# Kernel optimization log

Measured on AMD Instinct MI355X. Metric: run time of the kernel, lower is better.

## Reference

```python
import jax, jax.numpy as jnp
import numpy as np

S, B_BOX, C = 7, 2, 20
LAMBDA_COORD = 5.0
LAMBDA_NOOBJ = 0.5


def _iou(b1, b2):
    # b1, b2: [..., 4] in (cx, cy, w, h) format
    area1 = b1[..., 2] * b1[..., 3]
    area2 = b2[..., 2] * b2[..., 3]
    max_left = jnp.maximum(b1[..., 0] - b1[..., 2] / 2, b2[..., 0] - b2[..., 2] / 2)
    min_right = jnp.minimum(b1[..., 0] + b1[..., 2] / 2, b2[..., 0] + b2[..., 2] / 2)
    max_top = jnp.maximum(b1[..., 1] - b1[..., 3] / 2, b2[..., 1] - b2[..., 3] / 2)
    min_bottom = jnp.minimum(b1[..., 1] + b1[..., 3] / 2, b2[..., 1] + b2[..., 3] / 2)
    iw = jnp.maximum(min_right - max_left, 0.0)
    ih = jnp.maximum(min_bottom - max_top, 0.0)
    inter = iw * ih
    union = area1 + area2 - inter
    return jnp.where(inter > 0.0, inter / union, 0.0)


def setup_inputs() -> dict:
    key = jax.random.key(0)
    k1, k2, k3 = jax.random.split(key, 3)
    batch = 16384
    shape = (batch, S, S, C + 5 * B_BOX)  # [..., 30]
    pred = jax.random.uniform(k1, shape, dtype=jnp.float32)
    target = jax.random.uniform(k2, shape, dtype=jnp.float32)
    # objectness flag must be exactly 1.0 to trigger the obj branch
    obj_flag = jax.random.bernoulli(k3, 0.3, shape[:-1]).astype(jnp.float32)
    target = target.at[..., 0].set(obj_flag)
    return {"pred": pred, "target": target}


def reference(pred, target):
    batch = pred.shape[0]
    pred = pred.reshape(-1, S, S, C + 5 * B_BOX)
    target = target.reshape(-1, S, S, C + 5 * B_BOX)

    obj = (target[..., 0] == 1.0)          # [b,S,S] bool
    obj_f = obj.astype(pred.dtype)
    noobj_f = 1.0 - obj_f

    gt = target[..., 1:5]
    box1 = pred[..., 1:5]                   # predictor 1 box
    box2 = target[..., 6:10]                # NOTE: original code uses target's 2nd box
    iou1 = jax.lax.stop_gradient(_iou(box1, gt))
    iou2 = jax.lax.stop_gradient(_iou(box2, gt))
    resp1 = iou1 > iou2                     # predictor 1 responsible (strict >)
    r1 = resp1[..., None]

    # coord losses (responsible predictor)
    pxy = jnp.where(r1, pred[..., 1:3], pred[..., 6:8])
    txy = jnp.where(r1, target[..., 1:3], target[..., 6:8])
    pwh = jnp.where(r1, pred[..., 3:5], pred[..., 8:10])
    twh = jnp.where(r1, target[..., 3:5], target[..., 8:10])
    cell_xy = jnp.sum((pxy - txy) ** 2, axis=-1)
    cell_wh = jnp.sum((jnp.sqrt(pwh) - jnp.sqrt(twh)) ** 2, axis=-1)

    # obj confidence loss: responsible conf vs its iou
    conf_resp = jnp.where(resp1, pred[..., 0], pred[..., 5])
    iou_resp = jnp.where(resp1, iou1, iou2)
    cell_obj = (conf_resp - iou_resp) ** 2

    # noobj: non-responsible conf in obj cells; both confs in empty cells
    conf_other = jnp.where(resp1, pred[..., 5], pred[..., 0])
    cell_noobj_obj = conf_other ** 2
    cell_noobj_empty = pred[..., 0] ** 2 + pred[..., 5] ** 2

    cell_class = jnp.sum((pred[..., 10:] - target[..., 10:]) ** 2, axis=-1)

    loss_coord_xy = LAMBDA_COORD * jnp.sum(obj_f * cell_xy)
    loss_coord_wh = LAMBDA_COORD * jnp.sum(obj_f * cell_wh)
    loss_obj = jnp.sum(obj_f * cell_obj)
    loss_noobj = LAMBDA_NOOBJ * (jnp.sum(obj_f * cell_noobj_obj) + jnp.sum(noobj_f * cell_noobj_empty))
    loss_class = jnp.sum(obj_f * cell_class)
    loss = loss_coord_xy + loss_coord_wh + loss_obj + loss_noobj + loss_class

    bs = jnp.asarray(batch, pred.dtype)
    return ((loss_coord_xy + loss_coord_wh) / bs,
            loss_obj / bs,
            loss_noobj / bs,
            loss_class / bs,
            loss / bs)
```

## Files before the change

kernel.cpp:

```cpp
#include <hip/hip_runtime.h>

#define NCH 30
#define CPB 128
#define THREADS 256
#define GRID 1280

__device__ __forceinline__ float iou_fn(float x1, float y1, float w1, float h1,
                                        float x2, float y2, float w2, float h2) {
    float a1 = w1 * h1, a2 = w2 * h2;
    float left  = fmaxf(x1 - w1 * 0.5f, x2 - w2 * 0.5f);
    float right = fminf(x1 + w1 * 0.5f, x2 + w2 * 0.5f);
    float top   = fmaxf(y1 - h1 * 0.5f, y2 - h2 * 0.5f);
    float bot   = fminf(y1 + h1 * 0.5f, y2 + h2 * 0.5f);
    float iw = fmaxf(right - left, 0.0f);
    float ih = fmaxf(bot - top, 0.0f);
    float inter = iw * ih;
    float uni = a1 + a2 - inter;
    return (inter > 0.0f) ? (inter / uni) : 0.0f;
}

__global__ __launch_bounds__(THREADS) void yolo_main(
        const float* __restrict__ pred, const float* __restrict__ targ,
        float4* __restrict__ partials, int n_cells) {
    __shared__ float sp[CPB * NCH];
    __shared__ float st[CPB * NCH];

    const int tid = threadIdx.x;
    const int nchunks = (n_cells + CPB - 1) / CPB;
    const long long total_floats = (long long)n_cells * NCH;

    float coord = 0.f, lobj = 0.f, lnoobj = 0.f, lclass = 0.f;

    for (int c = blockIdx.x; c < nchunks; c += gridDim.x) {
        const long long base = (long long)c * (CPB * NCH);
        const long long rem = total_floats - base;
        const int nflt = rem < (long long)(CPB * NCH) ? (int)rem : (CPB * NCH);
        const int n4 = nflt >> 2;

        const float4* p4 = reinterpret_cast<const float4*>(pred + base);
        const float4* t4 = reinterpret_cast<const float4*>(targ + base);
        float4* sp4 = reinterpret_cast<float4*>(sp);
        float4* st4 = reinterpret_cast<float4*>(st);
        for (int i = tid; i < n4; i += THREADS) {
            float4 a = p4[i];
            float4 b = t4[i];
            sp4[i] = a;
            st4[i] = b;
        }
        for (int i = (n4 << 2) + tid; i < nflt; i += THREADS) {
            sp[i] = pred[base + i];
            st[i] = targ[base + i];
        }
        __syncthreads();

        if (tid < CPB) {
            long long cell = (long long)c * CPB + tid;
            if (cell < n_cells) {
                const float* p = sp + tid * NCH;
                const float* t = st + tid * NCH;

                float obj_f = (t[0] == 1.0f) ? 1.0f : 0.0f;

                float iou1 = iou_fn(p[1], p[2], p[3], p[4], t[1], t[2], t[3], t[4]);
                float iou2 = iou_fn(t[6], t[7], t[8], t[9], t[1], t[2], t[3], t[4]);
                bool r = iou1 > iou2;

                float px = r ? p[1] : p[6], py = r ? p[2] : p[7];
                float pw = r ? p[3] : p[8], ph = r ? p[4] : p[9];
                float tx = r ? t[1] : t[6], ty = r ? t[2] : t[7];
                float tw = r ? t[3] : t[8], th = r ? t[4] : t[9];

                float dx = px - tx, dy = py - ty;
                float cxy = dx * dx + dy * dy;
                float swv = sqrtf(pw) - sqrtf(tw), shv = sqrtf(ph) - sqrtf(th);
                float cwh = swv * swv + shv * shv;

                float conf_resp  = r ? p[0] : p[5];
                float iou_resp   = r ? iou1 : iou2;
                float conf_other = r ? p[5] : p[0];
                float dconf = conf_resp - iou_resp;

                coord  += obj_f * (cxy + cwh);
                lobj   += obj_f * dconf * dconf;
                lnoobj += obj_f * conf_other * conf_other
                        + (1.0f - obj_f) * (p[0] * p[0] + p[5] * p[5]);

                float cls = 0.0f;
#pragma unroll
                for (int i = 10; i < NCH; i++) { float e = p[i] - t[i]; cls += e * e; }
                lclass += obj_f * cls;
            }
        }
        __syncthreads();
    }

#pragma unroll
    for (int off = 32; off > 0; off >>= 1) {
        coord  += __shfl_down(coord, off);
        lobj   += __shfl_down(lobj, off);
        lnoobj += __shfl_down(lnoobj, off);
        lclass += __shfl_down(lclass, off);
    }

    __shared__ float red[4][4];
    int lane = tid & 63;
    int wid  = tid >> 6;
    if (lane == 0) {
        red[wid][0] = coord; red[wid][1] = lobj;
        red[wid][2] = lnoobj; red[wid][3] = lclass;
    }
    __syncthreads();
    if (tid == 0) {
        float s0 = 0.f, s1 = 0.f, s2 = 0.f, s3 = 0.f;
        for (int w = 0; w < 4; w++) {
            s0 += red[w][0]; s1 += red[w][1];
            s2 += red[w][2]; s3 += red[w][3];
        }
        partials[blockIdx.x] = make_float4(s0, s1, s2, s3);
    }
}

__global__ __launch_bounds__(THREADS) void yolo_reduce(
        const float4* __restrict__ partials, int nparts,
        float* __restrict__ out, double inv_bs) {
    double s0 = 0.0, s1 = 0.0, s2 = 0.0, s3 = 0.0;
    for (int i = threadIdx.x; i < nparts; i += THREADS) {
        float4 v = partials[i];
        s0 += (double)v.x; s1 += (double)v.y;
        s2 += (double)v.z; s3 += (double)v.w;
    }
#pragma unroll
    for (int off = 32; off > 0; off >>= 1) {
        s0 += __shfl_down(s0, off);
        s1 += __shfl_down(s1, off);
        s2 += __shfl_down(s2, off);
        s3 += __shfl_down(s3, off);
    }
    __shared__ double red[4][4];
    int lane = threadIdx.x & 63;
    int wid  = threadIdx.x >> 6;
    if (lane == 0) {
        red[wid][0] = s0; red[wid][1] = s1;
        red[wid][2] = s2; red[wid][3] = s3;
    }
    __syncthreads();
    if (threadIdx.x == 0) {
        double a0 = 0, a1 = 0, a2 = 0, a3 = 0;
        for (int w = 0; w < 4; w++) {
            a0 += red[w][0]; a1 += red[w][1];
            a2 += red[w][2]; a3 += red[w][3];
        }
        double c  = a0 * 5.0 * inv_bs;
        double o  = a1 * inv_bs;
        double n  = a2 * 0.5 * inv_bs;
        double cl = a3 * inv_bs;
        out[0] = (float)c;
        out[1] = (float)o;
        out[2] = (float)n;
        out[3] = (float)cl;
        out[4] = (float)(c + o + n + cl);
    }
}

extern "C" void kernel_launch(void* const* d_in, const int* in_sizes, int n_in,
                              void* d_out, int out_size, void* d_ws, size_t ws_size,
                              hipStream_t stream) {
    const float* pred = (const float*)d_in[0];
    const float* targ = (const float*)d_in[1];
    float* out = (float*)d_out;
    float4* partials = (float4*)d_ws;

    int n_cells = in_sizes[0] / NCH;
    int batch   = n_cells / 49;
    int nchunks = (n_cells + CPB - 1) / CPB;
    int grid    = nchunks < GRID ? nchunks : GRID;

    yolo_main<<<grid, THREADS, 0, stream>>>(pred, targ, partials, n_cells);
    yolo_reduce<<<1, THREADS, 0, stream>>>(partials, grid, out, 1.0 / (double)batch);
}
```

Measured before the change: 205.5 us.

## Software-pipeline global loads through registers with all threads computing cells

```diff
diff --git a/kernel.cpp b/kernel.cpp
--- a/kernel.cpp
+++ b/kernel.cpp
@@ -1,9 +1,10 @@
 #include <hip/hip_runtime.h>
 
 #define NCH 30
-#define CPB 128
+#define F2PC 15
+#define CPB 256
 #define THREADS 256
-#define GRID 1280
+#define GRID 512
 
 __device__ __forceinline__ float iou_fn(float x1, float y1, float w1, float h1,
                                         float x2, float y2, float w2, float h2) {
@@ -19,79 +20,110 @@
     return (inter > 0.0f) ? (inter / uni) : 0.0f;
 }
 
+__device__ __forceinline__ void cell_losses(const float* p, const float* t,
+                                            float& coord, float& lobj,
+                                            float& lnoobj, float& lclass) {
+    float obj_f = (t[0] == 1.0f) ? 1.0f : 0.0f;
+
+    float iou1 = iou_fn(p[1], p[2], p[3], p[4], t[1], t[2], t[3], t[4]);
+    float iou2 = iou_fn(t[6], t[7], t[8], t[9], t[1], t[2], t[3], t[4]);
+    bool r = iou1 > iou2;
+
+    float px = r ? p[1] : p[6], py = r ? p[2] : p[7];
+    float pw = r ? p[3] : p[8], ph = r ? p[4] : p[9];
+    float tx = r ? t[1] : t[6], ty = r ? t[2] : t[7];
+    float tw = r ? t[3] : t[8], th = r ? t[4] : t[9];
+
+    float dx = px - tx, dy = py - ty;
+    float cxy = dx * dx + dy * dy;
+    float swv = sqrtf(pw) - sqrtf(tw), shv = sqrtf(ph) - sqrtf(th);
+    float cwh = swv * swv + shv * shv;
+
+    float conf_resp  = r ? p[0] : p[5];
+    float iou_resp   = r ? iou1 : iou2;
+    float conf_other = r ? p[5] : p[0];
+    float dconf = conf_resp - iou_resp;
+
+    coord  += obj_f * (cxy + cwh);
+    lobj   += obj_f * dconf * dconf;
+    lnoobj += obj_f * conf_other * conf_other
+            + (1.0f - obj_f) * (p[0] * p[0] + p[5] * p[5]);
+
+    float cls = 0.0f;
+#pragma unroll
+    for (int i = 10; i < NCH; i++) { float e = p[i] - t[i]; cls += e * e; }
+    lclass += obj_f * cls;
+}
+
 __global__ __launch_bounds__(THREADS) void yolo_main(
-        const float* __restrict__ pred, const float* __restrict__ targ,
-        float4* __restrict__ partials, int n_cells) {
-    __shared__ float sp[CPB * NCH];
-    __shared__ float st[CPB * NCH];
+        const float2* __restrict__ pred2, const float2* __restrict__ targ2,
+        float4* __restrict__ partials, int nchunks_full, int n_cells) {
+    __shared__ float2 sp[CPB * F2PC];
+    __shared__ float2 st[CPB * F2PC];
 
     const int tid = threadIdx.x;
-    const int nchunks = (n_cells + CPB - 1) / CPB;
-    const long long total_floats = (long long)n_cells * NCH;
-
     float coord = 0.f, lobj = 0.f, lnoobj = 0.f, lclass = 0.f;
 
-    for (int c = blockIdx.x; c < nchunks; c += gridDim.x) {
-        const long long base = (long long)c * (CPB * NCH);
-        const long long rem = total_floats - base;
-        const int nflt = rem < (long long)(CPB * NCH) ? (int)rem : (CPB * NCH);
-        const int n4 = nflt >> 2;
-
-        const float4* p4 = reinterpret_cast<const float4*>(pred + base);
-        const float4* t4 = reinterpret_cast<const float4*>(targ + base);
-        float4* sp4 = reinterpret_cast<float4*>(sp);
-        float4* st4 = reinterpret_cast<float4*>(st);
-        for (int i = tid; i < n4; i += THREADS) {
-            float4 a = p4[i];
-            float4 b = t4[i];
-            sp4[i] = a;
-            st4[i] = b;
-        }
-        for (int i = (n4 << 2) + tid; i < nflt; i += THREADS) {
-            sp[i] = pred[base + i];
-            st[i] = targ[base + i];
-        }
+    float2 rp[F2PC], rt[F2PC];
+
+    int c = blockIdx.x;
+    bool have = c < nchunks_full;
+    if (have) {
+        const long long b = (long long)c * (CPB * F2PC);
+#pragma unroll
+        for (int k = 0; k < F2PC; k++) {
+            rp[k] = pred2[b + tid + k * THREADS];
+            rt[k] = targ2[b + tid + k * THREADS];
+        }
+    }
+
+    while (have) {
+        int cn = c + gridDim.x;
+        bool have_n = cn < nchunks_full;
+
         __syncthreads();
-
-        if (tid < CPB) {
-            long long cell = (long long)c * CPB + tid;
-            if (cell < n_cells) {
-                const float* p = sp + tid * NCH;
-                const float* t = st + tid * NCH;
-
-                float obj_f = (t[0] == 1.0f) ? 1.0f : 0.0f;
-
-                float iou1 = iou_fn(p[1], p[2], p[3], p[4], t[1], t[2], t[3], t[4]);
-                float iou2 = iou_fn(t[6], t[7], t[8], t[9], t[1], t[2], t[3], t[4]);
-                bool r = iou1 > iou2;
-
-                float px = r ? p[1] : p[6], py = r ? p[2] : p[7];
-                float pw = r ? p[3] : p[8], ph = r ? p[4] : p[9];
-                float tx = r ? t[1] : t[6], ty = r ? t[2] : t[7];
-                float tw = r ? t[3] : t[8], th = r ? t[4] : t[9];
-
-                float dx = px - tx, dy = py - ty;
-                float cxy = dx * dx + dy * dy;
-                float swv = sqrtf(pw) - sqrtf(tw), shv = sqrtf(ph) - sqrtf(th);
-                float cwh = swv * swv + shv * shv;
-
-                float conf_resp  = r ? p[0] : p[5];
-                float iou_resp   = r ? iou1 : iou2;
-                float conf_other = r ? p[5] : p[0];
-                float dconf = conf_resp - iou_resp;
-
-                coord  += obj_f * (cxy + cwh);
-                lobj   += obj_f * dconf * dconf;
-                lnoobj += obj_f * conf_other * conf_other
-                        + (1.0f - obj_f) * (p[0] * p[0] + p[5] * p[5]);
-
-                float cls = 0.0f;
-#pragma unroll
-                for (int i = 10; i < NCH; i++) { float e = p[i] - t[i]; cls += e * e; }
-                lclass += obj_f * cls;
+#pragma unroll
+        for (int k = 0; k < F2PC; k++) {
+            sp[tid + k * THREADS] = rp[k];
+            st[tid + k * THREADS] = rt[k];
+        }
+        __syncthreads();
+
+        if (have_n) {
+            const long long b = (long long)cn * (CPB * F2PC);
+#pragma unroll
+            for (int k = 0; k < F2PC; k++) {
+                rp[k] = pred2[b + tid + k * THREADS];
+                rt[k] = targ2[b + tid + k * THREADS];
             }
         }
-        __syncthreads();
+
+        {
+            float p[NCH], t[NCH];
+            const float2* pp = sp + tid * F2PC;
+            const float2* tp = st + tid * F2PC;
+#pragma unroll
+            for (int k = 0; k < F2PC; k++) { float2 v = pp[k]; p[2 * k] = v.x; p[2 * k + 1] = v.y; }
+#pragma unroll
+            for (int k = 0; k < F2PC; k++) { float2 v = tp[k]; t[2 * k] = v.x; t[2 * k + 1] = v.y; }
+            cell_losses(p, t, coord, lobj, lnoobj, lclass);
+        }
+
+        c = cn; have = have_n;
+    }
+
+    if (blockIdx.x == 0) {
+        int cell = nchunks_full * CPB + tid;
+        if (cell < n_cells) {
+            float p[NCH], t[NCH];
+            const float2* pp = pred2 + (long long)cell * F2PC;
+            const float2* tp = targ2 + (long long)cell * F2PC;
+#pragma unroll
+            for (int k = 0; k < F2PC; k++) { float2 v = pp[k]; p[2 * k] = v.x; p[2 * k + 1] = v.y; }
+#pragma unroll
+            for (int k = 0; k < F2PC; k++) { float2 v = tp[k]; t[2 * k] = v.x; t[2 * k + 1] = v.y; }
+            cell_losses(p, t, coord, lobj, lnoobj, lclass);
+        }
     }
 
 #pragma unroll
@@ -150,31 +182,32 @@
             a0 += red[w][0]; a1 += red[w][1];
             a2 += red[w][2]; a3 += red[w][3];
         }
-        double c  = a0 * 5.0 * inv_bs;
+        double cd = a0 * 5.0 * inv_bs;
         double o  = a1 * inv_bs;
         double n  = a2 * 0.5 * inv_bs;
         double cl = a3 * inv_bs;
-        out[0] = (float)c;
+        out[0] = (float)cd;
         out[1] = (float)o;
         out[2] = (float)n;
         out[3] = (float)cl;
-        out[4] = (float)(c + o + n + cl);
+        out[4] = (float)(cd + o + n + cl);
     }
 }
 
 extern "C" void kernel_launch(void* const* d_in, const int* in_sizes, int n_in,
                               void* d_out, int out_size, void* d_ws, size_t ws_size,
                               hipStream_t stream) {
-    const float* pred = (const float*)d_in[0];
-    const float* targ = (const float*)d_in[1];
+    const float2* pred2 = (const float2*)d_in[0];
+    const float2* targ2 = (const float2*)d_in[1];
     float* out = (float*)d_out;
     float4* partials = (float4*)d_ws;
 
     int n_cells = in_sizes[0] / NCH;
     int batch   = n_cells / 49;
-    int nchunks = (n_cells + CPB - 1) / CPB;
-    int grid    = nchunks < GRID ? nchunks : GRID;
-
-    yolo_main<<<grid, THREADS, 0, stream>>>(pred, targ, partials, n_cells);
+    int nchunks_full = n_cells / CPB;
+    int grid = nchunks_full < GRID ? nchunks_full : GRID;
+    if (grid < 1) grid = 1;
+
+    yolo_main<<<grid, THREADS, 0, stream>>>(pred2, targ2, partials, nchunks_full, n_cells);
     yolo_reduce<<<1, THREADS, 0, stream>>>(partials, grid, out, 1.0 / (double)batch);
 }
```

Measured after the change: 210.3 us. +2.3%, slower.
